# Kernel optimization log

Hardware: AMD Instinct MI355X
Metric: run time of the kernel (lower is better)

Reference implementation:

```python
import jax, jax.numpy as jnp
import numpy as np

EMB_DIM = 1024
N_HEADS = 16
HEAD_DIM = EMB_DIM // N_HEADS


def setup_inputs() -> dict:
    key = jax.random.key(0)
    k_x, k_qkv, k_w, k_b = jax.random.split(key, 4)
    x = jax.random.normal(k_x, (2, 2048, EMB_DIM), dtype=jnp.float32)
    # nn.Linear(emb_dim, 3*emb_dim, bias=False): weight [3E, E]; y = x @ W.T
    w_qkv = jax.random.normal(k_qkv, (3 * EMB_DIM, EMB_DIM), dtype=jnp.float32) * (EMB_DIM ** -0.5)
    # nn.Linear(emb_dim, emb_dim) with bias
    w_out = jax.random.normal(k_w, (EMB_DIM, EMB_DIM), dtype=jnp.float32) * (EMB_DIM ** -0.5)
    b_out = jax.random.normal(k_b, (EMB_DIM,), dtype=jnp.float32) * 0.01
    return {"x": x, "w_qkv": w_qkv, "w_out": w_out, "b_out": b_out}


def reference(x, w_qkv, w_out, b_out):
    B, S, E = x.shape
    H, D = N_HEADS, HEAD_DIM
    qkv = jnp.einsum('bse,fe->bsf', x, w_qkv)  # [B,S,3E]
    q, k, v = jnp.split(qkv, 3, axis=-1)
    # [B,S,E] -> [B,H,S,D]
    q = q.reshape(B, S, H, D).transpose(0, 2, 1, 3)
    k = k.reshape(B, S, H, D).transpose(0, 2, 1, 3)
    v = v.reshape(B, S, H, D).transpose(0, 2, 1, 3)
    scale = 1.0 / np.sqrt(D).astype(np.float32)
    scores = jnp.einsum('bhqd,bhkd->bhqk', q, k) * scale  # [B,H,S,S]
    causal = jnp.triu(jnp.ones((S, S), dtype=bool), k=1)
    scores = jnp.where(causal, -jnp.inf, scores)
    probs = jax.nn.softmax(scores, axis=-1)
    attn = jnp.einsum('bhqk,bhkd->bhqd', probs, v)  # [B,H,S,D]
    attn = attn.transpose(0, 2, 1, 3).reshape(B, S, E)
    return jnp.einsum('bse,fe->bsf', attn, w_out) + b_out
```

## Files before the change

kernel.cpp:

```cpp
#include <hip/hip_runtime.h>
#include <hip/hip_bf16.h>

#define EMB 1024
#define NH 16
#define HD 64
#define BATCH 2
#define SEQ 2048
#define MROWS (BATCH*SEQ)
#define F3 (3*EMB)

typedef __bf16 bf16;
typedef __attribute__((ext_vector_type(8))) __bf16 bf16x8;
typedef __attribute__((ext_vector_type(4))) __bf16 bf16x4;
typedef __attribute__((ext_vector_type(2))) __bf16 bf16x2;
typedef __attribute__((ext_vector_type(4))) float f32x4;
typedef __attribute__((ext_vector_type(16))) float f32x16;
typedef __attribute__((ext_vector_type(2))) unsigned int u32x2;

typedef const __attribute__((address_space(1))) void* gptr_t;
typedef __attribute__((address_space(3))) void* lptr_t;
#define GLDS16(g, l) __builtin_amdgcn_global_load_lds((gptr_t)(g), (lptr_t)(l), 16, 0, 0)

__device__ inline bf16 tobf(float f) {
    union { __hip_bfloat16 h; bf16 b; } cv;
    cv.h = __float2bfloat16(f);
    return cv.b;
}

__device__ inline float fexp2(float x) {
#if __has_builtin(__builtin_amdgcn_exp2f)
    return __builtin_amdgcn_exp2f(x);
#else
    return exp2f(x);
#endif
}

__device__ inline void plswap(unsigned& a, unsigned& b) {
#if __has_builtin(__builtin_amdgcn_permlane32_swap)
    u32x2 r = __builtin_amdgcn_permlane32_swap(a, b, false, false);
    a = r[0]; b = r[1];
#else
    unsigned pa = (unsigned)__shfl_xor((int)a, 32, 64);
    unsigned pb = (unsigned)__shfl_xor((int)b, 32, 64);
    bool hi = (threadIdx.x & 32) != 0;
    unsigned na = hi ? pb : a;
    unsigned nb = hi ? b : pa;
    a = na; b = nb;
#endif
}
__device__ inline void plswapf(float& a, float& b) {
    unsigned ua = __builtin_bit_cast(unsigned, a), ub = __builtin_bit_cast(unsigned, b);
    plswap(ua, ub);
    a = __builtin_bit_cast(float, ua); b = __builtin_bit_cast(float, ub);
}
__device__ inline unsigned pack2(float x, float y) {
    bf16x2 t; t[0] = (bf16)x; t[1] = (bf16)y;
    return __builtin_bit_cast(unsigned, t);
}

__global__ __launch_bounds__(256) void cvt_f32_bf16(const float* __restrict__ in,
                                                    bf16* __restrict__ out, int n) {
    int i = (blockIdx.x * 256 + threadIdx.x) * 4;
    if (i >= n) return;
    const float4 v = *reinterpret_cast<const float4*>(in + i);
    bf16x4 o;
    o[0] = tobf(v.x); o[1] = tobf(v.y); o[2] = tobf(v.z); o[3] = tobf(v.w);
    *reinterpret_cast<bf16x4*>(out + i) = o;
}

__global__ __launch_bounds__(256) void gemm_qkv(const bf16* __restrict__ A,
                                                const bf16* __restrict__ Bw,
                                                bf16* __restrict__ qb,
                                                bf16* __restrict__ kb,
                                                bf16* __restrict__ vt) {
    const int K = 1024;
    __shared__ alignas(16) bf16 Alds[128 * 32];
    __shared__ alignas(16) bf16 Blds[128 * 32];
    const int tid = threadIdx.x;
    const int w = tid >> 6, l = tid & 63;
    const int m0 = blockIdx.y * 128, n0 = blockIdx.x * 128;
    const int wr = w >> 1, wc = w & 1;

    f32x4 acc[4][4];
#pragma unroll
    for (int mi = 0; mi < 4; ++mi)
#pragma unroll
        for (int ni = 0; ni < 4; ++ni)
            acc[mi][ni] = f32x4{0.f, 0.f, 0.f, 0.f};

    const int srow = l >> 2;
    const int scol = (l & 3) * 8;
    const bf16* Abase = A + (size_t)m0 * K;
    const bf16* Bbase = Bw + (size_t)n0 * K;

    for (int k0 = 0; k0 < K; k0 += 32) {
#pragma unroll
        for (int i = 0; i < 2; ++i) {
            int chunk = w * 2 + i;
            int row = chunk * 16 + srow;
            GLDS16(Abase + (size_t)row * K + k0 + scol, &Alds[chunk * 512]);
            GLDS16(Bbase + (size_t)row * K + k0 + scol, &Blds[chunk * 512]);
        }
        __syncthreads();
        bf16x8 af[4], bfr[4];
#pragma unroll
        for (int mi = 0; mi < 4; ++mi)
            af[mi] = *reinterpret_cast<const bf16x8*>(
                &Alds[(wr * 64 + mi * 16 + (l & 15)) * 32 + (l >> 4) * 8]);
#pragma unroll
        for (int ni = 0; ni < 4; ++ni)
            bfr[ni] = *reinterpret_cast<const bf16x8*>(
                &Blds[(wc * 64 + ni * 16 + (l & 15)) * 32 + (l >> 4) * 8]);
#pragma unroll
        for (int mi = 0; mi < 4; ++mi)
#pragma unroll
            for (int ni = 0; ni < 4; ++ni)
                acc[mi][ni] = __builtin_amdgcn_mfma_f32_16x16x32_bf16(
                    af[mi], bfr[ni], acc[mi][ni], 0, 0, 0);
        __syncthreads();
    }

    const int which = n0 >> 10;
#pragma unroll
    for (int mi = 0; mi < 4; ++mi) {
#pragma unroll
        for (int ni = 0; ni < 4; ++ni) {
            int fcol = n0 + wc * 64 + ni * 16 + (l & 15);
            int h = (fcol >> 6) & 15, d = fcol & 63;
            int mbase = m0 + wr * 64 + mi * 16 + (l >> 4) * 4;
            int b = mbase >> 11, s = mbase & 2047;
            int bh = b * NH + h;
            if (which == 2) {
                bf16x4 vv;
#pragma unroll
                for (int jj = 0; jj < 4; ++jj) vv[jj] = tobf(acc[mi][ni][jj]);
                *reinterpret_cast<bf16x4*>(&vt[((size_t)bh * HD + d) * SEQ + s]) = vv;
            } else if (which == 0) {
#pragma unroll
                for (int jj = 0; jj < 4; ++jj)
                    qb[((size_t)bh * SEQ + s + jj) * HD + d] = tobf(acc[mi][ni][jj] * 0.180336881f);
            } else {
#pragma unroll
                for (int jj = 0; jj < 4; ++jj)
                    kb[((size_t)bh * SEQ + s + jj) * HD + d] = tobf(acc[mi][ni][jj]);
            }
        }
    }
}

__global__ __launch_bounds__(512, 4) void attn_kernel(const bf16* __restrict__ qb,
                                                      const bf16* __restrict__ kb,
                                                      const bf16* __restrict__ vt,
                                                      bf16* __restrict__ ao) {
    __shared__ alignas(16) char SM[69632];
    bf16 (*Kl)[4096] = (bf16 (*)[4096])SM;
    bf16 (*Vl)[4096] = (bf16 (*)[4096])(SM + 32768);
    float* Msh = (float*)(SM + 65536);
    float* Rsh = (float*)(SM + 67584);
    float* Osh = (float*)SM;

    const int tid = threadIdx.x, w = tid >> 6, l = tid & 63;
    const int hi = l >> 5;
    const int qg = w & 3, kg = w >> 2;
    const int h = (int)(blockIdx.x >> 5);
    const int qt = (h < 8) ? (15 - h) : (h - 8);
    const int bh = blockIdx.x & 31;
    const int q0 = qt * 128;
    const bf16* Qp = qb + (size_t)bh * SEQ * HD;
    const bf16* Kp = kb + (size_t)bh * SEQ * HD;
    const bf16* Vp = vt + (size_t)bh * HD * SEQ;

    const int qa = q0 + qg * 32 + (l & 31);
    bf16x8 qf[4];
#pragma unroll
    for (int kk = 0; kk < 4; ++kk)
        qf[kk] = *reinterpret_cast<const bf16x8*>(&Qp[(size_t)qa * HD + kk * 16 + hi * 8]);

    f32x16 o[2];
#pragma unroll
    for (int t = 0; t < 2; ++t)
#pragma unroll
        for (int r = 0; r < 16; ++r) o[t][r] = 0.f;
    float m = -__builtin_inff(), rs = 0.f;

    const int sc = ((l & 7) ^ (l >> 3)) * 8;

#define STAGE(itp)                                                                  \
    do {                                                                            \
        int j_ = 2 * (itp) + kg;                                                    \
        int slot_ = j_ & 3;                                                         \
        int kv0_ = j_ * 64;                                                         \
        int r0_ = qg * 16 + (l >> 3);                                               \
        GLDS16(Kp + (size_t)(kv0_ + r0_) * HD + sc, &Kl[slot_][(qg * 16) * 64]);    \
        GLDS16(Kp + (size_t)(kv0_ + r0_ + 8) * HD + sc, &Kl[slot_][(qg * 16 + 8) * 64]); \
        GLDS16(Vp + (size_t)r0_ * SEQ + kv0_ + sc, &Vl[slot_][(qg * 16) * 64]);     \
        GLDS16(Vp + (size_t)(r0_ + 8) * SEQ + kv0_ + sc, &Vl[slot_][(qg * 16 + 8) * 64]); \
    } while (0)

    STAGE(0);
    __syncthreads();

    const int qminw = q0 + qg * 32;
    const int qmaxw = qminw + 31;

    for (int it = 0; it <= qt; ++it) {
        if (it < qt) STAGE(it + 1);
        const int j = 2 * it + kg;
        if (j * 64 <= qmaxw) {
            const int slot = j & 3;
            f32x16 st[2];
#pragma unroll
            for (int t = 0; t < 2; ++t) {
#pragma unroll
                for (int r = 0; r < 16; ++r) st[t][r] = 0.f;
                int row = t * 32 + (l & 31);
                int rsw = (row & 7) << 3;
#pragma unroll
                for (int kk = 0; kk < 4; ++kk) {
                    bf16x8 kf = *reinterpret_cast<const bf16x8*>(
                        &Kl[slot][row * 64 + ((kk * 16 + hi * 8) ^ rsw)]);
                    st[t] = __builtin_amdgcn_mfma_f32_32x32x16_bf16(kf, qf[kk], st[t], 0, 0, 0);
                }
            }
            if (j * 64 + 63 > qminw) {
#pragma unroll
                for (int t = 0; t < 2; ++t)
#pragma unroll
                    for (int r = 0; r < 16; ++r) {
                        int kv = j * 64 + t * 32 + 8 * (r >> 2) + 4 * hi + (r & 3);
                        if (kv > qa) st[t][r] = -__builtin_inff();
                    }
            }
            float red[8];
#pragma unroll
            for (int r = 0; r < 8; ++r)
                red[r] = fmaxf(fmaxf(st[0][r], st[0][r + 8]), fmaxf(st[1][r], st[1][r + 8]));
            float pm = fmaxf(fmaxf(fmaxf(red[0], red[1]), fmaxf(red[2], red[3])),
                             fmaxf(fmaxf(red[4], red[5]), fmaxf(red[6], red[7])));
            float pa_ = pm, pb_ = pm;
            plswapf(pa_, pb_);
            pm = fmaxf(pa_, pb_);
            if (!__all(pm <= m + 8.f)) {
                float mn = fmaxf(m, pm);
                float al = fexp2(m - mn);
#pragma unroll
                for (int t = 0; t < 2; ++t)
#pragma unroll
                    for (int r = 0; r < 16; ++r) o[t][r] *= al;
                rs *= al;
                m = mn;
            }
#pragma unroll
            for (int t = 0; t < 2; ++t)
#pragma unroll
                for (int r = 0; r < 16; ++r) {
                    float p = fexp2(st[t][r] - m);
                    st[t][r] = p;
                    rs += p;
                }
#pragma unroll
            for (int t = 0; t < 2; ++t) {
                unsigned Ag[4], Bg[4];
#pragma unroll
                for (int g = 0; g < 4; ++g) {
                    Ag[g] = pack2(st[t][4 * g + 0], st[t][4 * g + 1]);
                    Bg[g] = pack2(st[t][4 * g + 2], st[t][4 * g + 3]);
                }
#pragma unroll
                for (int k2 = 0; k2 < 2; ++k2) {
                    unsigned w0 = Ag[2 * k2], w2 = Ag[2 * k2 + 1];
                    plswap(w0, w2);
                    unsigned w1 = Bg[2 * k2], w3 = Bg[2 * k2 + 1];
                    plswap(w1, w3);
                    union { unsigned u[4]; bf16x8 v; } pf;
                    pf.u[0] = w0; pf.u[1] = w1; pf.u[2] = w2; pf.u[3] = w3;
                    const int kk = 2 * t + k2;
#pragma unroll
                    for (int dt = 0; dt < 2; ++dt) {
                        int row = dt * 32 + (l & 31);
                        bf16x8 vf = *reinterpret_cast<const bf16x8*>(
                            &Vl[slot][row * 64 + ((kk * 16 + hi * 8) ^ ((row & 7) << 3))]);
                        o[dt] = __builtin_amdgcn_mfma_f32_32x32x16_bf16(vf, pf.v, o[dt], 0, 0, 0);
                    }
                }
            }
        }
        __syncthreads();
    }

    float rlo = rs, rhi = rs;
    plswapf(rlo, rhi);
    const float rfull = rlo + rhi;
    Msh[w * 64 + l] = m;
    Rsh[w * 64 + l] = rfull;
    if (kg == 1) {
        float* dst = Osh + (size_t)(qg * 64 + l) * 32;
#pragma unroll
        for (int c = 0; c < 8; ++c) {
            f32x4 tch;
#pragma unroll
            for (int i = 0; i < 4; ++i) tch[i] = o[c >> 2][(c & 3) * 4 + i];
            *reinterpret_cast<f32x4*>(dst + (c ^ (l & 7)) * 4) = tch;
        }
    }
    __syncthreads();
    if (kg == 0) {
        const float mb = Msh[(w + 4) * 64 + l];
        const float rb = Rsh[(w + 4) * 64 + l];
        const float mstar = fmaxf(m, mb);
        const float sa = fexp2(m - mstar), sb = fexp2(mb - mstar);
        const float inv = 1.f / (rfull * sa + rb * sb);
        const float* src = Osh + (size_t)(qg * 64 + l) * 32;
        const int b = bh >> 4, hh = bh & 15;
#pragma unroll
        for (int c = 0; c < 8; ++c) {
            f32x4 ob = *reinterpret_cast<const f32x4*>(src + (c ^ (l & 7)) * 4);
            bf16x4 ov;
#pragma unroll
            for (int i = 0; i < 4; ++i)
                ov[i] = (bf16)((o[c >> 2][(c & 3) * 4 + i] * sa + ob[i] * sb) * inv);
            int d0 = (c >> 2) * 32 + 8 * (c & 3) + 4 * hi;
            *reinterpret_cast<bf16x4*>(&ao[((size_t)b * SEQ + qa) * EMB + hh * HD + d0]) = ov;
        }
    }
#undef STAGE
}

__global__ __launch_bounds__(256) void gemm_out(const bf16* __restrict__ A,
                                                const bf16* __restrict__ Bw,
                                                float* __restrict__ out,
                                                const float* __restrict__ bias) {
    const int K = 1024;
    __shared__ alignas(16) bf16 Alds[128 * 32];
    __shared__ alignas(16) bf16 Blds[128 * 32];
    const int tid = threadIdx.x;
    const int w = tid >> 6, l = tid & 63;
    const int m0 = blockIdx.y * 128, n0 = blockIdx.x * 128;
    const int wr = w >> 1, wc = w & 1;

    f32x4 acc[4][4];
#pragma unroll
    for (int mi = 0; mi < 4; ++mi)
#pragma unroll
        for (int ni = 0; ni < 4; ++ni)
            acc[mi][ni] = f32x4{0.f, 0.f, 0.f, 0.f};

    const int srow = l >> 2;
    const int scol = (l & 3) * 8;
    const bf16* Abase = A + (size_t)m0 * K;
    const bf16* Bbase = Bw + (size_t)n0 * K;

    for (int k0 = 0; k0 < K; k0 += 32) {
#pragma unroll
        for (int i = 0; i < 2; ++i) {
            int chunk = w * 2 + i;
            int row = chunk * 16 + srow;
            GLDS16(Abase + (size_t)row * K + k0 + scol, &Alds[chunk * 512]);
            GLDS16(Bbase + (size_t)row * K + k0 + scol, &Blds[chunk * 512]);
        }
        __syncthreads();
        bf16x8 af[4], bfr[4];
#pragma unroll
        for (int mi = 0; mi < 4; ++mi)
            af[mi] = *reinterpret_cast<const bf16x8*>(
                &Alds[(wr * 64 + mi * 16 + (l & 15)) * 32 + (l >> 4) * 8]);
#pragma unroll
        for (int ni = 0; ni < 4; ++ni)
            bfr[ni] = *reinterpret_cast<const bf16x8*>(
                &Blds[(wc * 64 + ni * 16 + (l & 15)) * 32 + (l >> 4) * 8]);
#pragma unroll
        for (int mi = 0; mi < 4; ++mi)
#pragma unroll
            for (int ni = 0; ni < 4; ++ni)
                acc[mi][ni] = __builtin_amdgcn_mfma_f32_16x16x32_bf16(
                    af[mi], bfr[ni], acc[mi][ni], 0, 0, 0);
        __syncthreads();
    }

#pragma unroll
    for (int mi = 0; mi < 4; ++mi) {
#pragma unroll
        for (int ni = 0; ni < 4; ++ni) {
            int fcol = n0 + wc * 64 + ni * 16 + (l & 15);
            float bv = bias[fcol];
#pragma unroll
            for (int jj = 0; jj < 4; ++jj) {
                int m = m0 + wr * 64 + mi * 16 + (l >> 4) * 4 + jj;
                out[(size_t)m * EMB + fcol] = acc[mi][ni][jj] + bv;
            }
        }
    }
}

extern "C" void kernel_launch(void* const* d_in, const int* in_sizes, int n_in,
                              void* d_out, int out_size, void* d_ws, size_t ws_size,
                              hipStream_t stream) {
    const float* x     = (const float*)d_in[0];
    const float* w_qkv = (const float*)d_in[1];
    const float* w_out = (const float*)d_in[2];
    const float* b_out = (const float*)d_in[3];
    float* out = (float*)d_out;

    char* ws = (char*)d_ws;
    bf16* xb    = (bf16*)(ws);
    bf16* wqkvb = (bf16*)(ws + ((size_t)8 << 20));
    bf16* woutb = (bf16*)(ws + ((size_t)14 << 20));
    bf16* qb    = (bf16*)(ws + ((size_t)16 << 20));
    bf16* kb    = (bf16*)(ws + ((size_t)24 << 20));
    bf16* vt    = (bf16*)(ws + ((size_t)32 << 20));
    bf16* ab    = (bf16*)(ws + ((size_t)40 << 20));

    cvt_f32_bf16<<<4096, 256, 0, stream>>>(x, xb, MROWS * EMB);
    cvt_f32_bf16<<<3072, 256, 0, stream>>>(w_qkv, wqkvb, F3 * EMB);
    cvt_f32_bf16<<<1024, 256, 0, stream>>>(w_out, woutb, EMB * EMB);
    gemm_qkv<<<dim3(F3 / 128, MROWS / 128), 256, 0, stream>>>(xb, wqkvb, qb, kb, vt);
    attn_kernel<<<512, 512, 0, stream>>>(qb, kb, vt, ab);
    gemm_out<<<dim3(EMB / 128, MROWS / 128), 256, 0, stream>>>(ab, woutb, out, b_out);
}
```

Baseline: 178.4 us.

## Fuse conversion launches, raise MFMA priority in attention, shrink out-GEMM M tile

Merges the three f32-to-bf16 conversion launches into one kernel that picks its source buffer by index range, removing two launches. Wraps the QK and PV MFMA sections of the attention kernel in s_setprio so the scheduler favors matrix issue across waves. Halves the out-projection GEMM tile to 64x128, giving each wave a 64x32 slice and launching twice as many blocks (512) to fill more CUs. The smaller tile lowers per-block reuse of the weight tile.

```diff
diff --git a/kernel.cpp b/kernel.cpp
--- a/kernel.cpp
+++ b/kernel.cpp
@@ -58,14 +58,26 @@
     return __builtin_bit_cast(unsigned, t);
 }
 
-__global__ __launch_bounds__(256) void cvt_f32_bf16(const float* __restrict__ in,
-                                                    bf16* __restrict__ out, int n) {
+#define N1 (MROWS*EMB)
+#define N2 (F3*EMB)
+#define N3 (EMB*EMB)
+__global__ __launch_bounds__(256) void cvt_all(const float* __restrict__ x,
+                                               const float* __restrict__ wq,
+                                               const float* __restrict__ wo,
+                                               bf16* __restrict__ xb,
+                                               bf16* __restrict__ wqb,
+                                               bf16* __restrict__ wob) {
     int i = (blockIdx.x * 256 + threadIdx.x) * 4;
-    if (i >= n) return;
-    const float4 v = *reinterpret_cast<const float4*>(in + i);
+    const float* src;
+    bf16* dst;
+    int off;
+    if (i < N1)           { src = x;  dst = xb;  off = i; }
+    else if (i < N1 + N2) { src = wq; dst = wqb; off = i - N1; }
+    else                  { src = wo; dst = wob; off = i - N1 - N2; }
+    const float4 v = *reinterpret_cast<const float4*>(src + off);
     bf16x4 o;
     o[0] = tobf(v.x); o[1] = tobf(v.y); o[2] = tobf(v.z); o[3] = tobf(v.w);
-    *reinterpret_cast<bf16x4*>(out + i) = o;
+    *reinterpret_cast<bf16x4*>(dst + off) = o;
 }
 
 __global__ __launch_bounds__(256) void gemm_qkv(const bf16* __restrict__ A,
@@ -209,6 +221,7 @@
         if (j * 64 <= qmaxw) {
             const int slot = j & 3;
             f32x16 st[2];
+            __builtin_amdgcn_s_setprio(1);
 #pragma unroll
             for (int t = 0; t < 2; ++t) {
 #pragma unroll
@@ -222,6 +235,7 @@
                     st[t] = __builtin_amdgcn_mfma_f32_32x32x16_bf16(kf, qf[kk], st[t], 0, 0, 0);
                 }
             }
+            __builtin_amdgcn_s_setprio(0);
             if (j * 64 + 63 > qminw) {
 #pragma unroll
                 for (int t = 0; t < 2; ++t)
@@ -266,6 +280,7 @@
                     Ag[g] = pack2(st[t][4 * g + 0], st[t][4 * g + 1]);
                     Bg[g] = pack2(st[t][4 * g + 2], st[t][4 * g + 3]);
                 }
+                __builtin_amdgcn_s_setprio(1);
 #pragma unroll
                 for (int k2 = 0; k2 < 2; ++k2) {
                     unsigned w0 = Ag[2 * k2], w2 = Ag[2 * k2 + 1];
@@ -283,6 +298,7 @@
                         o[dt] = __builtin_amdgcn_mfma_f32_32x32x16_bf16(vf, pf.v, o[dt], 0, 0, 0);
                     }
                 }
+                __builtin_amdgcn_s_setprio(0);
             }
         }
         __syncthreads();
@@ -331,18 +347,17 @@
                                                 float* __restrict__ out,
                                                 const float* __restrict__ bias) {
     const int K = 1024;
-    __shared__ alignas(16) bf16 Alds[128 * 32];
+    __shared__ alignas(16) bf16 Alds[64 * 32];
     __shared__ alignas(16) bf16 Blds[128 * 32];
     const int tid = threadIdx.x;
     const int w = tid >> 6, l = tid & 63;
-    const int m0 = blockIdx.y * 128, n0 = blockIdx.x * 128;
-    const int wr = w >> 1, wc = w & 1;
-
-    f32x4 acc[4][4];
+    const int m0 = blockIdx.y * 64, n0 = blockIdx.x * 128;
+
+    f32x4 acc[4][2];
 #pragma unroll
     for (int mi = 0; mi < 4; ++mi)
 #pragma unroll
-        for (int ni = 0; ni < 4; ++ni)
+        for (int ni = 0; ni < 2; ++ni)
             acc[mi][ni] = f32x4{0.f, 0.f, 0.f, 0.f};
 
     const int srow = l >> 2;
@@ -351,27 +366,26 @@
     const bf16* Bbase = Bw + (size_t)n0 * K;
 
     for (int k0 = 0; k0 < K; k0 += 32) {
+        GLDS16(Abase + (size_t)(w * 16 + srow) * K + k0 + scol, &Alds[w * 512]);
 #pragma unroll
         for (int i = 0; i < 2; ++i) {
             int chunk = w * 2 + i;
-            int row = chunk * 16 + srow;
-            GLDS16(Abase + (size_t)row * K + k0 + scol, &Alds[chunk * 512]);
-            GLDS16(Bbase + (size_t)row * K + k0 + scol, &Blds[chunk * 512]);
+            GLDS16(Bbase + (size_t)(chunk * 16 + srow) * K + k0 + scol, &Blds[chunk * 512]);
         }
         __syncthreads();
-        bf16x8 af[4], bfr[4];
+        bf16x8 af[4], bfr[2];
 #pragma unroll
         for (int mi = 0; mi < 4; ++mi)
             af[mi] = *reinterpret_cast<const bf16x8*>(
-                &Alds[(wr * 64 + mi * 16 + (l & 15)) * 32 + (l >> 4) * 8]);
-#pragma unroll
-        for (int ni = 0; ni < 4; ++ni)
+                &Alds[(mi * 16 + (l & 15)) * 32 + (l >> 4) * 8]);
+#pragma unroll
+        for (int ni = 0; ni < 2; ++ni)
             bfr[ni] = *reinterpret_cast<const bf16x8*>(
-                &Blds[(wc * 64 + ni * 16 + (l & 15)) * 32 + (l >> 4) * 8]);
+                &Blds[(w * 32 + ni * 16 + (l & 15)) * 32 + (l >> 4) * 8]);
 #pragma unroll
         for (int mi = 0; mi < 4; ++mi)
 #pragma unroll
-            for (int ni = 0; ni < 4; ++ni)
+            for (int ni = 0; ni < 2; ++ni)
                 acc[mi][ni] = __builtin_amdgcn_mfma_f32_16x16x32_bf16(
                     af[mi], bfr[ni], acc[mi][ni], 0, 0, 0);
         __syncthreads();
@@ -380,12 +394,12 @@
 #pragma unroll
     for (int mi = 0; mi < 4; ++mi) {
 #pragma unroll
-        for (int ni = 0; ni < 4; ++ni) {
-            int fcol = n0 + wc * 64 + ni * 16 + (l & 15);
+        for (int ni = 0; ni < 2; ++ni) {
+            int fcol = n0 + w * 32 + ni * 16 + (l & 15);
             float bv = bias[fcol];
 #pragma unroll
             for (int jj = 0; jj < 4; ++jj) {
-                int m = m0 + wr * 64 + mi * 16 + (l >> 4) * 4 + jj;
+                int m = m0 + mi * 16 + (l >> 4) * 4 + jj;
                 out[(size_t)m * EMB + fcol] = acc[mi][ni][jj] + bv;
             }
         }
@@ -410,10 +424,8 @@
     bf16* vt    = (bf16*)(ws + ((size_t)32 << 20));
     bf16* ab    = (bf16*)(ws + ((size_t)40 << 20));
 
-    cvt_f32_bf16<<<4096, 256, 0, stream>>>(x, xb, MROWS * EMB);
-    cvt_f32_bf16<<<3072, 256, 0, stream>>>(w_qkv, wqkvb, F3 * EMB);
-    cvt_f32_bf16<<<1024, 256, 0, stream>>>(w_out, woutb, EMB * EMB);
+    cvt_all<<<(N1 + N2 + N3) / 1024, 256, 0, stream>>>(x, w_qkv, w_out, xb, wqkvb, woutb);
     gemm_qkv<<<dim3(F3 / 128, MROWS / 128), 256, 0, stream>>>(xb, wqkvb, qb, kb, vt);
     attn_kernel<<<512, 512, 0, stream>>>(qb, kb, vt, ab);
-    gemm_out<<<dim3(EMB / 128, MROWS / 128), 256, 0, stream>>>(ab, woutb, out, b_out);
-}
+    gemm_out<<<dim3(EMB / 128, MROWS / 64), 256, 0, stream>>>(ab, woutb, out, b_out);
+}
```

Result: faster. 170.2 us (-4.6%).
